# Kernel optimization log

Measured on AMD Instinct MI355X. Metric: run time of the kernel, lower is better.

## Reference

```python
import jax, jax.numpy as jnp
import numpy as np

B, N, IN_DIM, OUT_DIM, H = 8, 1024, 256, 256, 4
HD = OUT_DIM // H  # head_dim = 64
NEG = -1e9
EPS = 1e-5


def setup_inputs() -> dict:
    key = jax.random.key(0)
    ks = jax.random.split(key, 9)
    h = jax.random.normal(ks[0], (B, N, IN_DIM), dtype=jnp.float32)
    adj = jax.random.randint(ks[1], (N, N), 0, 2, dtype=jnp.int32)
    adj = adj.at[jnp.arange(N), jnp.arange(N)].set(1)  # self loops so no empty rows
    s = 1.0 / np.sqrt(IN_DIM)
    W = jax.random.uniform(ks[2], (H, IN_DIM, HD), jnp.float32, -s, s)
    sa = 1.0 / np.sqrt(2 * HD)
    a1 = jax.random.uniform(ks[3], (H, HD), jnp.float32, -sa, sa)
    a2 = jax.random.uniform(ks[4], (H, HD), jnp.float32, -sa, sa)
    sp = 1.0 / np.sqrt(OUT_DIM)
    proj_w = jax.random.uniform(ks[5], (OUT_DIM, OUT_DIM), jnp.float32, -sp, sp)
    proj_b = jax.random.uniform(ks[6], (OUT_DIM,), jnp.float32, -sp, sp)
    gamma = jnp.ones((OUT_DIM,), jnp.float32)
    beta = jnp.zeros((OUT_DIM,), jnp.float32)
    return {"h": h, "adj": adj, "W": W, "a1": a1, "a2": a2,
            "proj_w": proj_w, "proj_b": proj_b, "gamma": gamma, "beta": beta}


def reference(h, adj, W, a1, a2, proj_w, proj_b, gamma, beta):
    # Wh: [B,H,N,HD]
    Wh = jnp.einsum('bni,hid->bhnd', h, W)
    # Decompose a([Wh_i || Wh_j]) = a1.Wh_i + a2.Wh_j (same math as concat+linear)
    si = jnp.einsum('bhnd,hd->bhn', Wh, a1)  # [B,H,N]
    sj = jnp.einsum('bhnd,hd->bhn', Wh, a2)
    e = jax.nn.leaky_relu(si[:, :, :, None] + sj[:, :, None, :], 0.2)  # [B,H,N,N]
    mask = (adj == 0)  # [N,N]
    e = jnp.where(mask[None, None], NEG, e)
    alpha = jax.nn.softmax(e, axis=-1)
    out = jnp.einsum('bhnm,bhmd->bhnd', alpha, Wh)  # [B,H,N,HD]
    h_multi = out.transpose(0, 2, 1, 3).reshape(B, N, OUT_DIM)  # concat heads
    h_out = jnp.einsum('bnd,od->bno', h_multi, proj_w) + proj_b
    h_out = h_out + h  # residual (in_dim == out_dim)
    mu = jnp.mean(h_out, axis=-1, keepdims=True)
    var = jnp.mean(jnp.square(h_out - mu), axis=-1, keepdims=True)
    return (h_out - mu) * jax.lax.rsqrt(var + EPS) * gamma + beta
```

## Files before the change

### kernel.cpp

```cpp
#include <hip/hip_runtime.h>
#include <hip/hip_bf16.h>

#define NN 1024
#define LOG2E 1.44269504088896f

typedef __attribute__((ext_vector_type(8))) short short8;
typedef __attribute__((ext_vector_type(4))) short short4e;
typedef __attribute__((ext_vector_type(4))) float floatx4;
typedef __attribute__((ext_vector_type(4))) int intx4;
typedef __attribute__((ext_vector_type(2))) int intx2;

static __device__ __forceinline__ unsigned pk2(float f0, float f1) {
    unsigned u0 = __float_as_uint(f0) + 0x8000u;
    unsigned u1 = __float_as_uint(f1) + 0x8000u;
    return __builtin_amdgcn_perm(u1, u0, 0x07060302u);
}
static __device__ __forceinline__ short8 pk8(floatx4 v0, floatx4 v1) {
    union { intx4 i; short8 s; } u;
    u.i[0] = (int)pk2(v0[0], v0[1]); u.i[1] = (int)pk2(v0[2], v0[3]);
    u.i[2] = (int)pk2(v1[0], v1[1]); u.i[3] = (int)pk2(v1[2], v1[3]);
    return u.s;
}

__global__ __launch_bounds__(256) void prep_kernel(
    const float* __restrict__ W, const float* __restrict__ proj_w,
    const int* __restrict__ adj,
    __hip_bfloat16* __restrict__ WTb,
    __hip_bfloat16* __restrict__ pwb,
    unsigned* __restrict__ adjm)
{
    int blk = blockIdx.x, t = threadIdx.x;
    if (blk < 16) {
        int o = blk * 16 + (t >> 4);
        int hh = o >> 6, d = o & 63;
        #pragma unroll
        for (int kk = 0; kk < 16; ++kk) {
            int k = (t & 15) + 16 * kk;
            WTb[(size_t)o * 256 + k] = __float2bfloat16(W[((size_t)hh * 256 + k) * 64 + d]);
        }
    } else if (blk < 32) {
        size_t base = (size_t)(blk - 16) * 4096 + (size_t)t * 16;
        #pragma unroll
        for (int k = 0; k < 16; k += 8) {
            floatx4 v0 = *(const floatx4*)(proj_w + base + k);
            floatx4 v1 = *(const floatx4*)(proj_w + base + k + 4);
            *(short8*)(pwb + base + k) = pk8(v0, v1);
        }
    } else {
        int n = (blk - 32) * 8 + (t >> 5);
        int wd = t & 31;
        const int* arow = adj + (size_t)n * NN + wd * 32;
        unsigned bits = 0;
        #pragma unroll
        for (int j4 = 0; j4 < 8; ++j4) {
            intx4 v = *(const intx4*)(arow + j4 * 4);
            #pragma unroll
            for (int j = 0; j < 4; ++j) if (v[j] != 0) bits |= (1u << (j4 * 4 + j));
        }
        adjm[(size_t)n * 32 + wd] = bits;
    }
}

__global__ __launch_bounds__(256) void wh_kernel(
    const float* __restrict__ h,
    const __hip_bfloat16* __restrict__ WTb,
    const float* __restrict__ a1, const float* __restrict__ a2,
    __hip_bfloat16* __restrict__ WhT,
    float* __restrict__ si, float* __restrict__ sj)
{
    int t = threadIdx.x;
    int w = t >> 6, l = t & 63;
    int rl = l & 15, q = l >> 4;
    int r0 = blockIdx.x * 16;
    int bb = r0 >> 10, n0 = r0 & 1023;

    __shared__ __align__(16) __hip_bfloat16 bst[4][16][264];
    __shared__ float redsi[4][4][16];
    __shared__ float redsj[4][4][16];

    short8 af[8];
    const float* Arow = h + (size_t)(r0 + rl) * 256 + q * 8;
    #pragma unroll
    for (int k0 = 0; k0 < 8; ++k0) {
        floatx4 v0 = *(const floatx4*)(Arow + k0 * 32);
        floatx4 v1 = *(const floatx4*)(Arow + k0 * 32 + 4);
        af[k0] = pk8(v0, v1);
    }

    short8 sreg[8], nreg[8];
    {
        const __hip_bfloat16* src = WTb + (size_t)w * 16 * 256;
        #pragma unroll
        for (int k = 0; k < 8; ++k) sreg[k] = *(const short8*)(src + k * 512 + l * 8);
    }

    #pragma unroll
    for (int j = 0; j < 4; ++j) {
        if (j < 3) {
            const __hip_bfloat16* src = WTb + (size_t)(w + 4 * (j + 1)) * 16 * 256;
            #pragma unroll
            for (int k = 0; k < 8; ++k) nreg[k] = *(const short8*)(src + k * 512 + l * 8);
        }
        #pragma unroll
        for (int k = 0; k < 8; ++k)
            *(short8*)(&bst[w][k * 2 + (l >> 5)][(l & 31) * 8]) = sreg[k];
        floatx4 acc = {0.f, 0.f, 0.f, 0.f};
        #pragma unroll
        for (int k0 = 0; k0 < 8; ++k0) {
            short8 bf = *(const short8*)(&bst[w][rl][q * 8 + k0 * 32]);
            acc = __builtin_amdgcn_mfma_f32_16x16x32_bf16(af[k0], bf, acc, 0, 0, 0);
        }

        intx2 pr;
        pr[0] = (int)pk2(acc[0], acc[1]);
        pr[1] = (int)pk2(acc[2], acc[3]);
        *(intx2*)(WhT + ((size_t)(bb * 4 + j) * 64 + w * 16 + rl) * NN + n0 + q * 4) = pr;

        float av1 = a1[j * 64 + w * 16 + rl] * LOG2E;
        float av2 = a2[j * 64 + w * 16 + rl] * LOG2E;
        #pragma unroll
        for (int i = 0; i < 4; ++i) {
            float p1 = acc[i] * av1, p2 = acc[i] * av2;
            #pragma unroll
            for (int off = 1; off < 16; off <<= 1) {
                p1 += __shfl_xor(p1, off, 64);
                p2 += __shfl_xor(p2, off, 64);
            }
            if (rl == 0) { redsi[w][j][q * 4 + i] = p1; redsj[w][j][q * 4 + i] = p2; }
        }
        #pragma unroll
        for (int z = 0; z < 8; ++z) sreg[z] = nreg[z];
    }
    __syncthreads();

    if (t < 64) {
        int head = t >> 4, row = t & 15;
        si[(size_t)(bb * 4 + head) * NN + n0 + row] =
            redsi[0][head][row] + redsi[1][head][row] + redsi[2][head][row] + redsi[3][head][row];
    } else if (t < 128) {
        int u = t - 64;
        int head = u >> 4, row = u & 15;
        sj[(size_t)(bb * 4 + head) * NN + n0 + row] =
            redsj[0][head][row] + redsj[1][head][row] + redsj[2][head][row] + redsj[3][head][row];
    }
}

__global__ __launch_bounds__(256) void attn_proj_kernel(
    const unsigned* __restrict__ adjm,
    const __hip_bfloat16* __restrict__ WhT,
    const float* __restrict__ si, const float* __restrict__ sj,
    const __hip_bfloat16* __restrict__ pwb,
    const float* __restrict__ h,
    const float* __restrict__ proj_b, const float* __restrict__ gamma,
    const float* __restrict__ beta,
    float* __restrict__ out)
{
    __shared__ __align__(16) char smem[46592];
    auto bst   = reinterpret_cast<__hip_bfloat16 (*)[64][72]>(smem);
    auto pl    = reinterpret_cast<__hip_bfloat16 (*)[16][72]>(smem + 36864);
    auto rinvs = reinterpret_cast<float (*)[16]>(smem + 46080);
    auto pbst  = reinterpret_cast<__hip_bfloat16 (*)[16][264]>(smem);
    auto hm    = reinterpret_cast<__hip_bfloat16 (*)[264]>(smem + 36864);
    auto red   = reinterpret_cast<float (*)[4][16]>(smem + 45312);

    int bx = blockIdx.x, t = threadIdx.x;
    int w = t >> 6, l = t & 63;
    int rl = l & 15, q = l >> 4;
    int b = bx >> 6, n0 = (bx & 63) * 16;
    int bh = b * 4 + w;
    int r0 = bx * 16;

    int r = l >> 2, cg = l & 3;
    float sii = si[(size_t)bh * NN + n0 + r];
    const float* sjr = sj + (size_t)bh * NN;
    const unsigned* amrow = adjm + (size_t)(n0 + r) * 32;

    float lsum = 0.f;
    floatx4 acc[4] = { {0,0,0,0}, {0,0,0,0}, {0,0,0,0}, {0,0,0,0} };

    const __hip_bfloat16* Bsrc = WhT + (size_t)bh * 64 * NN;

    short8 sreg[8], nreg[8];
    #pragma unroll
    for (int k = 0; k < 8; ++k)
        sreg[k] = *(const short8*)(Bsrc + (size_t)(k * 8 + (l >> 3)) * NN + (l & 7) * 8);

    #pragma unroll
    for (int it = 0; it < 16; ++it) {
        int m0 = it * 64;
        if (it < 15) {
            int m1 = m0 + 64;
            #pragma unroll
            for (int k = 0; k < 8; ++k)
                nreg[k] = *(const short8*)(Bsrc + (size_t)(k * 8 + (l >> 3)) * NN + m1 + (l & 7) * 8);
        }
        {
            int mb = m0 + cg * 16;
            unsigned bits = amrow[(m0 >> 5) + (cg >> 1)] >> ((cg & 1) * 16);
            #pragma unroll
            for (int c4 = 0; c4 < 4; ++c4) {
                floatx4 s4 = *(const floatx4*)(sjr + mb + c4 * 4);
                float pv[4];
                #pragma unroll
                for (int k = 0; k < 4; ++k) {
                    float x = sii + s4[k];
                    x = fmaxf(x, 0.2f * x);
                    x = ((bits >> (c4 * 4 + k)) & 1u) ? x : -1e9f;
                    pv[k] = exp2f(x);
                    lsum += pv[k];
                }
                intx2 two;
                two[0] = (int)pk2(pv[0], pv[1]);
                two[1] = (int)pk2(pv[2], pv[3]);
                *(intx2*)(&pl[w][r][cg * 16 + c4 * 4]) = two;
            }
        }
        #pragma unroll
        for (int k = 0; k < 8; ++k)
            *(short8*)(&bst[w][k * 8 + (l >> 3)][(l & 7) * 8]) = sreg[k];
        #pragma unroll
        for (int ks = 0; ks < 2; ++ks) {
            short8 afr = *(const short8*)(&pl[w][rl][q * 8 + ks * 32]);
            #pragma unroll
            for (int dt = 0; dt < 4; ++dt) {
                short8 bfr = *(const short8*)(&bst[w][dt * 16 + rl][q * 8 + ks * 32]);
                acc[dt] = __builtin_amdgcn_mfma_f32_16x16x32_bf16(afr, bfr, acc[dt], 0, 0, 0);
            }
        }
        #pragma unroll
        for (int z = 0; z < 8; ++z) sreg[z] = nreg[z];
    }

    lsum += __shfl_xor(lsum, 1, 64);
    lsum += __shfl_xor(lsum, 2, 64);
    if (cg == 0) rinvs[w][r] = 1.f / lsum;
    float riv[4];
    #pragma unroll
    for (int i = 0; i < 4; ++i) riv[i] = rinvs[w][q * 4 + i];

    short8 psreg[8], pnreg[8];
    {
        const __hip_bfloat16* src = pwb + (size_t)w * 16 * 256;
        #pragma unroll
        for (int k = 0; k < 8; ++k) psreg[k] = *(const short8*)(src + k * 512 + l * 8);
    }

    __syncthreads();
    #pragma unroll
    for (int dt = 0; dt < 4; ++dt) {
        #pragma unroll
        for (int i = 0; i < 4; ++i) {
            unsigned uv = (__float_as_uint(acc[dt][i] * riv[i]) + 0x8000u) >> 16;
            hm[q * 4 + i][w * 64 + dt * 16 + rl] = __ushort_as_bfloat16((unsigned short)uv);
        }
    }
    __syncthreads();

    short8 paf[8];
    #pragma unroll
    for (int k0 = 0; k0 < 8; ++k0) paf[k0] = *(const short8*)(&hm[rl][q * 8 + k0 * 32]);

    floatx4 pacc[4];
    #pragma unroll
    for (int j = 0; j < 4; ++j) {
        if (j < 3) {
            const __hip_bfloat16* src = pwb + (size_t)(w + 4 * (j + 1)) * 16 * 256;
            #pragma unroll
            for (int k = 0; k < 8; ++k) pnreg[k] = *(const short8*)(src + k * 512 + l * 8);
        }
        #pragma unroll
        for (int k = 0; k < 8; ++k)
            *(short8*)(&pbst[w][k * 2 + (l >> 5)][(l & 31) * 8]) = psreg[k];
        floatx4 a = {0.f, 0.f, 0.f, 0.f};
        #pragma unroll
        for (int k0 = 0; k0 < 8; ++k0) {
            short8 bf = *(const short8*)(&pbst[w][rl][q * 8 + k0 * 32]);
            a = __builtin_amdgcn_mfma_f32_16x16x32_bf16(paf[k0], bf, a, 0, 0, 0);
        }
        pacc[j] = a;
        #pragma unroll
        for (int z = 0; z < 8; ++z) psreg[z] = pnreg[z];
    }

    float ps[4] = {0.f, 0.f, 0.f, 0.f};
    #pragma unroll
    for (int j = 0; j < 4; ++j) {
        int col = (w + j * 4) * 16 + rl;
        float pb = proj_b[col];
        #pragma unroll
        for (int i = 0; i < 4; ++i) {
            float v = pacc[j][i] + pb + h[(size_t)(r0 + q * 4 + i) * 256 + col];
            pacc[j][i] = v;
            ps[i] += v;
        }
    }
    #pragma unroll
    for (int i = 0; i < 4; ++i) {
        float s = ps[i];
        #pragma unroll
        for (int off = 1; off < 16; off <<= 1) s += __shfl_xor(s, off, 64);
        ps[i] = s;
    }
    if (rl == 0) {
        for (int i = 0; i < 4; ++i) red[0][w][q * 4 + i] = ps[i];
    }
    __syncthreads();
    float mu[4];
    #pragma unroll
    for (int i = 0; i < 4; ++i) {
        int row = q * 4 + i;
        mu[i] = (red[0][0][row] + red[0][1][row] + red[0][2][row] + red[0][3][row]) * (1.f / 256.f);
    }
    float vs[4] = {0.f, 0.f, 0.f, 0.f};
    #pragma unroll
    for (int j = 0; j < 4; ++j) {
        #pragma unroll
        for (int i = 0; i < 4; ++i) { float cv = pacc[j][i] - mu[i]; vs[i] += cv * cv; }
    }
    #pragma unroll
    for (int i = 0; i < 4; ++i) {
        float s = vs[i];
        #pragma unroll
        for (int off = 1; off < 16; off <<= 1) s += __shfl_xor(s, off, 64);
        vs[i] = s;
    }
    if (rl == 0) {
        for (int i = 0; i < 4; ++i) red[1][w][q * 4 + i] = vs[i];
    }
    __syncthreads();
    float rs[4];
    #pragma unroll
    for (int i = 0; i < 4; ++i) {
        int row = q * 4 + i;
        float var = (red[1][0][row] + red[1][1][row] + red[1][2][row] + red[1][3][row]) * (1.f / 256.f);
        rs[i] = rsqrtf(var + 1e-5f);
    }
    #pragma unroll
    for (int j = 0; j < 4; ++j) {
        int col = (w + j * 4) * 16 + rl;
        float g = gamma[col], be = beta[col];
        #pragma unroll
        for (int i = 0; i < 4; ++i)
            out[(size_t)(r0 + q * 4 + i) * 256 + col] = (pacc[j][i] - mu[i]) * rs[i] * g + be;
    }
}

extern "C" void kernel_launch(void* const* d_in, const int* in_sizes, int n_in,
                              void* d_out, int out_size, void* d_ws, size_t ws_size,
                              hipStream_t stream) {
    const float* h      = (const float*)d_in[0];
    const int*   adj    = (const int*)d_in[1];
    const float* W      = (const float*)d_in[2];
    const float* a1     = (const float*)d_in[3];
    const float* a2     = (const float*)d_in[4];
    const float* proj_w = (const float*)d_in[5];
    const float* proj_b = (const float*)d_in[6];
    const float* gamma  = (const float*)d_in[7];
    const float* beta   = (const float*)d_in[8];
    float* out = (float*)d_out;

    char* ws = (char*)d_ws;
    __hip_bfloat16* WhT = (__hip_bfloat16*)ws;   ws += (size_t)32 * 64 * NN * 2;
    __hip_bfloat16* WTb = (__hip_bfloat16*)ws;   ws += 256 * 256 * 2;
    __hip_bfloat16* pwb = (__hip_bfloat16*)ws;   ws += 256 * 256 * 2;
    float* si = (float*)ws;                      ws += (size_t)32 * NN * 4;
    float* sj = (float*)ws;                      ws += (size_t)32 * NN * 4;
    unsigned* adjm = (unsigned*)ws;              ws += (size_t)NN * 32 * 4;

    prep_kernel<<<160, 256, 0, stream>>>(W, proj_w, adj, WTb, pwb, adjm);
    wh_kernel<<<512, 256, 0, stream>>>(h, WTb, a1, a2, WhT, si, sj);
    attn_proj_kernel<<<512, 256, 0, stream>>>(adjm, WhT, si, sj, pwb, h, proj_b, gamma, beta, out);
}
```

Baseline: 122.1 us.

## Stream B tiles via global_load_lds into double-buffered XOR-swizzled LDS

Replaces the register-staged prefetch (global load to VGPRs, then ds_write) in both the Wh GEMM and attention kernels with direct global-to-LDS loads into a double-buffered, XOR-swizzled shared tile. This removes the VGPR staging and the explicit LDS stores, and the swizzle is meant to avoid bank conflicts on the MFMA operand reads. No explicit waitcnt or barrier is added between the async LDS fill and its consumption, so correctness depends on compiler-inserted vmcnt waits. Attention-kernel LDS grows to about 75KB, which may reduce occupancy.

Result: no change. 120.9 us (-1.0%).

```diff
diff --git a/kernel.cpp b/kernel.cpp
--- a/kernel.cpp
+++ b/kernel.cpp
@@ -5,7 +5,6 @@
 #define LOG2E 1.44269504088896f
 
 typedef __attribute__((ext_vector_type(8))) short short8;
-typedef __attribute__((ext_vector_type(4))) short short4e;
 typedef __attribute__((ext_vector_type(4))) float floatx4;
 typedef __attribute__((ext_vector_type(4))) int intx4;
 typedef __attribute__((ext_vector_type(2))) int intx2;
@@ -20,6 +19,11 @@
     u.i[0] = (int)pk2(v0[0], v0[1]); u.i[1] = (int)pk2(v0[2], v0[3]);
     u.i[2] = (int)pk2(v1[0], v1[1]); u.i[3] = (int)pk2(v1[2], v1[3]);
     return u.s;
+}
+static __device__ __forceinline__ void load_lds16(const void* gsrc, void* lds) {
+    __builtin_amdgcn_global_load_lds(
+        (const __attribute__((address_space(1))) void*)gsrc,
+        (__attribute__((address_space(3))) void*)lds, 16, 0, 0);
 }
 
 __global__ __launch_bounds__(256) void prep_kernel(
@@ -74,7 +78,7 @@
     int r0 = blockIdx.x * 16;
     int bb = r0 >> 10, n0 = r0 & 1023;
 
-    __shared__ __align__(16) __hip_bfloat16 bst[4][16][264];
+    __shared__ __align__(16) __hip_bfloat16 bst[4][2][4096];
     __shared__ float redsi[4][4][16];
     __shared__ float redsj[4][4][16];
 
@@ -87,27 +91,30 @@
         af[k0] = pk8(v0, v1);
     }
 
-    short8 sreg[8], nreg[8];
-    {
-        const __hip_bfloat16* src = WTb + (size_t)w * 16 * 256;
-        #pragma unroll
-        for (int k = 0; k < 8; ++k) sreg[k] = *(const short8*)(src + k * 512 + l * 8);
-    }
-
-    #pragma unroll
-    for (int j = 0; j < 4; ++j) {
+    #pragma unroll
+    for (int k = 0; k < 8; ++k) {
+        int row = k * 2 + (l >> 5);
+        int g = (l & 31) ^ (row & 7);
+        load_lds16(WTb + (size_t)w * 4096 + row * 256 + g * 8, &bst[w][0][k * 512]);
+    }
+
+    #pragma unroll
+    for (int j = 0; j < 4; ++j) {
+        int cur = j & 1;
         if (j < 3) {
-            const __hip_bfloat16* src = WTb + (size_t)(w + 4 * (j + 1)) * 16 * 256;
-            #pragma unroll
-            for (int k = 0; k < 8; ++k) nreg[k] = *(const short8*)(src + k * 512 + l * 8);
-        }
-        #pragma unroll
-        for (int k = 0; k < 8; ++k)
-            *(short8*)(&bst[w][k * 2 + (l >> 5)][(l & 31) * 8]) = sreg[k];
+            int ctn = w + 4 * (j + 1);
+            #pragma unroll
+            for (int k = 0; k < 8; ++k) {
+                int row = k * 2 + (l >> 5);
+                int g = (l & 31) ^ (row & 7);
+                load_lds16(WTb + (size_t)ctn * 4096 + row * 256 + g * 8, &bst[w][cur ^ 1][k * 512]);
+            }
+        }
         floatx4 acc = {0.f, 0.f, 0.f, 0.f};
         #pragma unroll
         for (int k0 = 0; k0 < 8; ++k0) {
-            short8 bf = *(const short8*)(&bst[w][rl][q * 8 + k0 * 32]);
+            int p = ((k0 << 2) + q) ^ (rl & 7);
+            short8 bf = *(const short8*)(&bst[w][cur][rl * 256 + p * 8]);
             acc = __builtin_amdgcn_mfma_f32_16x16x32_bf16(af[k0], bf, acc, 0, 0, 0);
         }
 
@@ -128,8 +135,6 @@
             }
             if (rl == 0) { redsi[w][j][q * 4 + i] = p1; redsj[w][j][q * 4 + i] = p2; }
         }
-        #pragma unroll
-        for (int z = 0; z < 8; ++z) sreg[z] = nreg[z];
     }
     __syncthreads();
 
@@ -155,13 +160,13 @@
     const float* __restrict__ beta,
     float* __restrict__ out)
 {
-    __shared__ __align__(16) char smem[46592];
-    auto bst   = reinterpret_cast<__hip_bfloat16 (*)[64][72]>(smem);
-    auto pl    = reinterpret_cast<__hip_bfloat16 (*)[16][72]>(smem + 36864);
-    auto rinvs = reinterpret_cast<float (*)[16]>(smem + 46080);
+    __shared__ __align__(16) char smem[75264];
+    auto bst   = reinterpret_cast<__hip_bfloat16 (*)[2][8192 / 2]>(smem);
+    auto pl    = reinterpret_cast<__hip_bfloat16 (*)[16][72]>(smem + 65536);
+    auto rinvs = reinterpret_cast<float (*)[16]>(smem + 74752);
     auto pbst  = reinterpret_cast<__hip_bfloat16 (*)[16][264]>(smem);
-    auto hm    = reinterpret_cast<__hip_bfloat16 (*)[264]>(smem + 36864);
-    auto red   = reinterpret_cast<float (*)[4][16]>(smem + 45312);
+    auto hm    = reinterpret_cast<__hip_bfloat16 (*)[264]>(smem + 65536);
+    auto red   = reinterpret_cast<float (*)[4][16]>(smem + 74752);
 
     int bx = blockIdx.x, t = threadIdx.x;
     int w = t >> 6, l = t & 63;
@@ -178,21 +183,24 @@
     float lsum = 0.f;
     floatx4 acc[4] = { {0,0,0,0}, {0,0,0,0}, {0,0,0,0}, {0,0,0,0} };
 
-    const __hip_bfloat16* Bsrc = WhT + (size_t)bh * 64 * NN;
-
-    short8 sreg[8], nreg[8];
+    const __hip_bfloat16* Bhead = WhT + (size_t)bh * 64 * NN;
+    int lrow = l >> 3;
+    int lgrp = (l & 7) ^ lrow;
+
     #pragma unroll
     for (int k = 0; k < 8; ++k)
-        sreg[k] = *(const short8*)(Bsrc + (size_t)(k * 8 + (l >> 3)) * NN + (l & 7) * 8);
+        load_lds16(Bhead + (size_t)(k * 8 + lrow) * NN + lgrp * 8, &bst[w][0][k * 512]);
 
     #pragma unroll
     for (int it = 0; it < 16; ++it) {
         int m0 = it * 64;
+        int cur = it & 1;
         if (it < 15) {
             int m1 = m0 + 64;
             #pragma unroll
             for (int k = 0; k < 8; ++k)
-                nreg[k] = *(const short8*)(Bsrc + (size_t)(k * 8 + (l >> 3)) * NN + m1 + (l & 7) * 8);
+                load_lds16(Bhead + (size_t)(k * 8 + lrow) * NN + m1 + lgrp * 8,
+                           &bst[w][cur ^ 1][k * 512]);
         }
         {
             int mb = m0 + cg * 16;
@@ -216,19 +224,15 @@
             }
         }
         #pragma unroll
-        for (int k = 0; k < 8; ++k)
-            *(short8*)(&bst[w][k * 8 + (l >> 3)][(l & 7) * 8]) = sreg[k];
-        #pragma unroll
         for (int ks = 0; ks < 2; ++ks) {
-            short8 afr = *(const short8*)(&pl[w][rl][q * 8 + ks * 32]);
+            short8 afr = *(const short8*)(&pl[w][rl][ks * 32 + q * 8]);
             #pragma unroll
             for (int dt = 0; dt < 4; ++dt) {
-                short8 bfr = *(const short8*)(&bst[w][dt * 16 + rl][q * 8 + ks * 32]);
+                int p = ((ks << 2) + q) ^ (rl & 7);
+                short8 bfr = *(const short8*)(&bst[w][cur][(dt * 16 + rl) * 64 + p * 8]);
                 acc[dt] = __builtin_amdgcn_mfma_f32_16x16x32_bf16(afr, bfr, acc[dt], 0, 0, 0);
             }
         }
-        #pragma unroll
-        for (int z = 0; z < 8; ++z) sreg[z] = nreg[z];
     }
 
     lsum += __shfl_xor(lsum, 1, 64);
```
